# Kernel tuning notes

Measured on AMD Instinct MI355X. Metric: run time of the kernel, lower is better.

The kernel has to match this reference:

```python
import jax, jax.numpy as jnp
import numpy as np

B, N, K = 4, 4096, 16
EPS = 1e-12


def setup_inputs() -> dict:
    key = jax.random.key(0)
    k1, k2, k3 = jax.random.split(key, 3)
    ori = jax.random.normal(k1, (B, N, 3), dtype=jnp.float32)
    # adversarial cloud = original + small perturbation (realistic attack setting)
    adv = ori + 0.05 * jax.random.normal(k2, (B, N, 3), dtype=jnp.float32)
    nrm = jax.random.normal(k3, (B, N, 3), dtype=jnp.float32)
    nrm = nrm / (jnp.linalg.norm(nrm, axis=-1, keepdims=True) + EPS)  # unit normals
    return {"ori_pcs": ori, "adv_pcs": adv, "ori_normals": nrm, "k": K}


def _sqdist(a, b):
    # a: [B,N,3], b: [B,M,3] -> [B,N,M] squared euclidean distances (GEMM form)
    return ((a * a).sum(-1)[:, :, None] + (b * b).sum(-1)[:, None, :]
            - 2.0 * jnp.einsum('bnd,bmd->bnm', a, b))


def _gather_rows(pts, idx):
    # pts: [B,M,3], idx: [B,...] int -> [B,...,3]
    return jax.vmap(lambda p, i: p[i])(pts, idx)


def _kappa(pc, normals, k):
    # curvature proxy: mean |<normalized offset to kNN, normal>| per point -> [B,N]
    d = _sqdist(pc, pc)                       # [B,N,N]
    _, idx = jax.lax.top_k(-d, k + 1)         # nearest k+1 (incl. self)
    idx = idx[..., 1:]                        # drop self -> [B,N,k]
    nn = _gather_rows(pc, idx)                # [B,N,k,3]
    vec = nn - pc[:, :, None, :]
    vec = vec / (jnp.linalg.norm(vec, axis=-1, keepdims=True) + EPS)
    return jnp.abs(jnp.einsum('bnkd,bnd->bnk', vec, normals)).mean(-1)


def reference(ori_pcs, adv_pcs, ori_normals, k):
    # curvature of the clean cloud
    kappa_ori = _kappa(ori_pcs, ori_normals, k)            # [B,N]
    # adv points borrow the normal of their nearest original point
    d = _sqdist(adv_pcs, ori_pcs)                          # [B,N,N]
    nn_idx = jnp.argmin(d, axis=-1)                        # [B,N]
    adv_normals = _gather_rows(ori_normals, nn_idx)        # [B,N,3]
    kappa_adv = _kappa(adv_pcs, adv_normals, k)            # [B,N]
    # std of curvature over points (torch.std -> unbiased, ddof=1)
    std_ori = jnp.std(kappa_ori, axis=1, ddof=1)           # [B]
    std_adv = jnp.std(kappa_adv, axis=1, ddof=1)           # [B]
    return jnp.mean(jnp.abs(std_adv - std_ori))
```

## Files before the change

kernel.cpp:

```cpp
#include <hip/hip_runtime.h>
#include <math.h>

#define B_ 4
#define N_ 4096
#define K_ 16
#define WAVES 8
#define QPB (WAVES*2)
#define BPB (N_/QPB)
#define INF __builtin_huge_valf()

__device__ __forceinline__ float dpp_shr1_f(float x) {
    return __int_as_float(__builtin_amdgcn_update_dpp(
        __float_as_int(x), __float_as_int(x), 0x111, 0xF, 0xF, false));
}
__device__ __forceinline__ int dpp_shr1_i(int x) {
    return __builtin_amdgcn_update_dpp(x, x, 0x111, 0xF, 0xF, false);
}
__device__ __forceinline__ float readlane_f(float x, int l) {
    return __int_as_float(__builtin_amdgcn_readlane(__float_as_int(x), l));
}

#if __has_builtin(__builtin_amdgcn_inverse_ballot_w64)
#define LANEBIT(m, lane) __builtin_amdgcn_inverse_ballot_w64(m)
#else
#define LANEBIT(m, lane) ((((m) >> (lane)) & 1ull) != 0)
#endif

__global__ __launch_bounds__(512, 6) void curv_argmin_kernel(
    const float* __restrict__ ori, const float* __restrict__ adv,
    int* __restrict__ nnidx)
{
    __shared__ float2 sxy[N_];
    __shared__ float  sz[N_];
    const int tid = threadIdx.x, lane = tid & 63, w = tid >> 6;
    const int b  = blockIdx.x >> 8;
    const int qb = (blockIdx.x & 255) * QPB;
    const float* ob = ori + (size_t)b * (N_*3);
    const float* ab = adv + (size_t)b * (N_*3);
    for (int k = 0; k < N_/512; ++k) {
        int j = k*512 + tid;
        sxy[j] = make_float2(ob[3*j+0], ob[3*j+1]);
        sz[j]  = ob[3*j+2];
    }
    __syncthreads();

    const int n0 = qb + w*2, n1 = n0 + 1;
    const float m2x0 = -2.f*ab[3*n0+0], m2y0 = -2.f*ab[3*n0+1], m2z0 = -2.f*ab[3*n0+2];
    const float m2x1 = -2.f*ab[3*n1+0], m2y1 = -2.f*ab[3*n1+1], m2z1 = -2.f*ab[3*n1+2];

    float dm0 = INF, dm1 = INF; int jm0 = 0, jm1 = 0;
    for (int t = 0; t < N_/64; ++t) {
        int j = t*64 + lane;
        float2 p = sxy[j]; float pz = sz[j];
        float pp = fmaf(pz,pz, fmaf(p.y,p.y, p.x*p.x));
        float r0 = fmaf(pz,m2z0, fmaf(p.y,m2y0, fmaf(p.x,m2x0, pp)));
        float r1 = fmaf(pz,m2z1, fmaf(p.y,m2y1, fmaf(p.x,m2x1, pp)));
        if (r0 < dm0) { dm0 = r0; jm0 = j; }
        if (r1 < dm1) { dm1 = r1; jm1 = j; }
    }
    for (int s = 1; s < 64; s <<= 1) {
        float o0 = __shfl_xor(dm0, s); int a0 = __shfl_xor(jm0, s);
        float o1 = __shfl_xor(dm1, s); int a1 = __shfl_xor(jm1, s);
        if (o0 < dm0 || (o0 == dm0 && a0 < jm0)) { dm0 = o0; jm0 = a0; }
        if (o1 < dm1 || (o1 == dm1 && a1 < jm1)) { dm1 = o1; jm1 = a1; }
    }
    if (lane == 0) { nnidx[b*N_+n0] = jm0; nnidx[b*N_+n1] = jm1; }
}

__global__ __launch_bounds__(512, 6) void curv_kappa_kernel(
    const float* __restrict__ ori, const float* __restrict__ adv,
    const float* __restrict__ nrm, const int* __restrict__ nnidx,
    double* __restrict__ acc)
{
    __shared__ float2 sxy[N_];
    __shared__ float  sz[N_];
    __shared__ double rs[WAVES], rss[WAVES];
    const int tid = threadIdx.x, lane = tid & 63, w = tid >> 6;
    const int blk = blockIdx.x;
    const int job = blk >> 10;
    const int b   = (blk >> 8) & 3;
    const int qb  = (blk & 255) * QPB;

    const float* pb = (job ? adv : ori) + (size_t)b*(N_*3);
    const float* nb = nrm + (size_t)b*(N_*3);
    for (int k = 0; k < N_/512; ++k) {
        int j = k*512 + tid;
        sxy[j] = make_float2(pb[3*j+0], pb[3*j+1]);
        sz[j]  = pb[3*j+2];
    }
    __syncthreads();

    const int n0 = qb + w*2, n1 = n0 + 1;
    const float2 q0 = sxy[n0]; const float q0z = sz[n0];
    const float2 q1 = sxy[n1]; const float q1z = sz[n1];
    const float m2x0 = -2.f*q0.x, m2y0 = -2.f*q0.y, m2z0 = -2.f*q0z;
    const float m2x1 = -2.f*q1.x, m2y1 = -2.f*q1.y, m2z1 = -2.f*q1z;

    int nn0 = n0, nn1 = n1;
    if (job) { nn0 = nnidx[b*N_+n0]; nn1 = nnidx[b*N_+n1]; }
    const float nx0 = nb[3*nn0+0], ny0 = nb[3*nn0+1], nz0 = nb[3*nn0+2];
    const float nx1 = nb[3*nn1+0], ny1 = nb[3*nn1+1], nz1 = nb[3*nn1+2];

    const int selfT = n0 >> 6;

    float r0, r1; int i0 = lane, i1 = lane;
    {
        float2 p = sxy[lane]; float pz = sz[lane];
        float pp = fmaf(pz,pz, fmaf(p.y,p.y, p.x*p.x));
        r0 = fmaf(pz,m2z0, fmaf(p.y,m2y0, fmaf(p.x,m2x0, pp)));
        r1 = fmaf(pz,m2z1, fmaf(p.y,m2y1, fmaf(p.x,m2x1, pp)));
        if (selfT == 0) {
            if (lane == n0) r0 = INF;
            if (lane == n1) r1 = INF;
        }
    }
    #pragma unroll
    for (int k = 2; k <= 64; k <<= 1) {
        #pragma unroll
        for (int j = k >> 1; j > 0; j >>= 1) {
            bool sel = ((lane & k) == 0) == ((lane & j) == 0);
            float o0 = __shfl_xor(r0, j); int a0 = __shfl_xor(i0, j);
            float o1 = __shfl_xor(r1, j); int a1 = __shfl_xor(i1, j);
            if ((o0 < r0) == sel) { r0 = o0; i0 = a0; }
            if ((o1 < r1) == sel) { r1 = o1; i1 = a1; }
        }
    }
    float sd0 = r0, sd1 = r1; int si0 = i0, si1 = i1;
    float tau0 = readlane_f(sd0, 15), tau1 = readlane_f(sd1, 15);
    const int selfL0 = n0 & 63, selfL1 = n1 & 63;

    for (int t = 1; t < N_/64; ++t) {
        int j = t*64 + lane;
        float2 p = sxy[j]; float pz = sz[j];
        float pp = fmaf(pz,pz, fmaf(p.y,p.y, p.x*p.x));
        float d0 = fmaf(pz,m2z0, fmaf(p.y,m2y0, fmaf(p.x,m2x0, pp)));
        float d1 = fmaf(pz,m2z1, fmaf(p.y,m2y1, fmaf(p.x,m2x1, pp)));
        if (t == selfT) {
            if (lane == selfL0) d0 = INF;
            if (lane == selfL1) d1 = INF;
        }
        unsigned long long m0 = __ballot(d0 < tau0);
        if (m0) {
            do {
                int src = __builtin_ctzll(m0); m0 &= m0 - 1;
                float v = readlane_f(d0, src);
                int  vi = t*64 + src;
                bool gt = (sd0 > v);
                unsigned long long mg = __ballot(gt);
                float usd = dpp_shr1_f(sd0); int usi = dpp_shr1_i(si0);
                bool pg = LANEBIT(mg << 1, lane);
                sd0 = gt ? (pg ? usd : v ) : sd0;
                si0 = gt ? (pg ? usi : vi) : si0;
            } while (m0);
            tau0 = readlane_f(sd0, 15);
        }
        unsigned long long m1 = __ballot(d1 < tau1);
        if (m1) {
            do {
                int src = __builtin_ctzll(m1); m1 &= m1 - 1;
                float v = readlane_f(d1, src);
                int  vi = t*64 + src;
                bool gt = (sd1 > v);
                unsigned long long mg = __ballot(gt);
                float usd = dpp_shr1_f(sd1); int usi = dpp_shr1_i(si1);
                bool pg = LANEBIT(mg << 1, lane);
                sd1 = gt ? (pg ? usd : v ) : sd1;
                si1 = gt ? (pg ? usi : vi) : si1;
            } while (m1);
            tau1 = readlane_f(sd1, 15);
        }
    }

    float tl0 = 0.0f, tl1 = 0.0f;
    if (lane < K_) {
        {
            float2 p = sxy[si0]; float pz = sz[si0];
            float vx = p.x - q0.x, vy = p.y - q0.y, vz = pz - q0z;
            float L  = sqrtf(vx*vx + vy*vy + vz*vz) + 1e-12f;
            tl0 = fabsf(vx*nx0 + vy*ny0 + vz*nz0) / L;
        }
        {
            float2 p = sxy[si1]; float pz = sz[si1];
            float vx = p.x - q1.x, vy = p.y - q1.y, vz = pz - q1z;
            float L  = sqrtf(vx*vx + vy*vy + vz*vz) + 1e-12f;
            tl1 = fabsf(vx*nx1 + vy*ny1 + vz*nz1) / L;
        }
    }
    tl0 += __shfl_xor(tl0, 1); tl0 += __shfl_xor(tl0, 2);
    tl0 += __shfl_xor(tl0, 4); tl0 += __shfl_xor(tl0, 8);
    tl1 += __shfl_xor(tl1, 1); tl1 += __shfl_xor(tl1, 2);
    tl1 += __shfl_xor(tl1, 4); tl1 += __shfl_xor(tl1, 8);

    if (lane == 0) {
        double k0 = (double)tl0 * (1.0/16.0);
        double k1 = (double)tl1 * (1.0/16.0);
        rs[w]  = k0 + k1;
        rss[w] = k0*k0 + k1*k1;
    }
    __syncthreads();
    if (tid == 0) {
        double s = 0.0, ss = 0.0;
        #pragma unroll
        for (int i = 0; i < WAVES; ++i) { s += rs[i]; ss += rss[i]; }
        int row = job*4 + b;
        atomicAdd(&acc[row*2+0], s);
        atomicAdd(&acc[row*2+1], ss);
    }
}

__global__ void curv_finalize_kernel(const double* __restrict__ acc,
                                     float* __restrict__ out)
{
    if (threadIdx.x == 0 && blockIdx.x == 0) {
        double st[8];
        #pragma unroll
        for (int r = 0; r < 8; ++r) {
            double s   = acc[2*r+0];
            double ss  = acc[2*r+1];
            double var = (ss - s*s / (double)N_) / (double)(N_ - 1);
            st[r] = var > 0.0 ? sqrt(var) : 0.0;
        }
        double o = 0.0;
        #pragma unroll
        for (int bb = 0; bb < 4; ++bb) o += fabs(st[4+bb] - st[bb]);
        out[0] = (float)(o * 0.25);
    }
}

extern "C" void kernel_launch(void* const* d_in, const int* in_sizes, int n_in,
                              void* d_out, int out_size, void* d_ws, size_t ws_size,
                              hipStream_t stream)
{
    const float* ori = (const float*)d_in[0];
    const float* adv = (const float*)d_in[1];
    const float* nrm = (const float*)d_in[2];
    double* acc   = (double*)d_ws;
    int*    nnidx = (int*)((char*)d_ws + 128);
    float*  out   = (float*)d_out;

    hipMemsetAsync(acc, 0, 16 * sizeof(double), stream);
    curv_argmin_kernel<<<dim3(B_ * BPB), 512, 0, stream>>>(ori, adv, nnidx);
    curv_kappa_kernel<<<dim3(2 * B_ * BPB), 512, 0, stream>>>(ori, adv, nrm, nnidx, acc);
    curv_finalize_kernel<<<1, 64, 0, stream>>>(acc, out);
}
```

Before: 117.3 us.

## Sort points by z and prune kNN/argmin tiles via z-bound early exit

Adds a counting-sort kernel that buckets both clouds by z coordinate into a workspace, carrying each point's original index. The argmin and kNN kernels then scan 64-point tiles outward from the query's own tile, using per-tile prefix/suffix z bounds to stop once no remaining tile can beat the current best or k-th distance. This is meant to skip most of the all-pairs distance work, at the cost of an extra kernel, a fixed z range assumption in bucketing (clamped, so only sort quality suffers), and a small slack term in the pruning test.

```diff
diff --git a/kernel.cpp b/kernel.cpp
--- a/kernel.cpp
+++ b/kernel.cpp
@@ -7,7 +7,9 @@
 #define WAVES 8
 #define QPB (WAVES*2)
 #define BPB (N_/QPB)
+#define NBUCK 512
 #define INF __builtin_huge_valf()
+#define SLACK 1e-4f
 
 __device__ __forceinline__ float dpp_shr1_f(float x) {
     return __int_as_float(__builtin_amdgcn_update_dpp(
@@ -19,100 +21,227 @@
 __device__ __forceinline__ float readlane_f(float x, int l) {
     return __int_as_float(__builtin_amdgcn_readlane(__float_as_int(x), l));
 }
-
 #if __has_builtin(__builtin_amdgcn_inverse_ballot_w64)
 #define LANEBIT(m, lane) __builtin_amdgcn_inverse_ballot_w64(m)
 #else
 #define LANEBIT(m, lane) ((((m) >> (lane)) & 1ull) != 0)
 #endif
 
+#define POPS(m, dd, sdv, siv, tauv, tbase)                                 \
+    if (m) {                                                               \
+        do {                                                               \
+            int src = __builtin_ctzll(m); m &= m - 1;                      \
+            float v = readlane_f(dd, src);                                 \
+            int  vi = (tbase) + src;                                       \
+            bool gt = (sdv > v);                                           \
+            unsigned long long mg = __ballot(gt);                          \
+            float usd = dpp_shr1_f(sdv); int usi = dpp_shr1_i(siv);        \
+            bool pg = LANEBIT(mg << 1, lane);                              \
+            sdv = gt ? (pg ? usd : v ) : sdv;                              \
+            siv = gt ? (pg ? usi : vi) : siv;                              \
+        } while (m);                                                       \
+        tauv = readlane_f(sdv, 15);                                        \
+    }
+
+__global__ __launch_bounds__(512) void sortz_kernel(
+    const float* __restrict__ ori, const float* __restrict__ adv,
+    float4* __restrict__ gs)
+{
+    __shared__ int hist[NBUCK];
+    __shared__ int base[NBUCK];
+    __shared__ unsigned short sbuck[N_];
+    const int tid = threadIdx.x;
+    const int set = blockIdx.x >> 2;
+    const int b   = blockIdx.x & 3;
+    const float* src = (set ? adv : ori) + (size_t)b * (N_*3);
+    float4* dst = gs + (size_t)blockIdx.x * N_;
+
+    hist[tid] = 0;
+    __syncthreads();
+    #pragma unroll
+    for (int k = 0; k < N_/512; ++k) {
+        int j = k*512 + tid;
+        float z = src[3*j+2];
+        int bu = (int)((z + 4.25f) * (NBUCK/8.5f));
+        bu = bu < 0 ? 0 : (bu > NBUCK-1 ? NBUCK-1 : bu);
+        sbuck[j] = (unsigned short)bu;
+        atomicAdd(&hist[bu], 1);
+    }
+    __syncthreads();
+    int v = hist[tid];
+    for (int s = 1; s < NBUCK; s <<= 1) {
+        base[tid] = v; __syncthreads();
+        if (tid >= s) v += base[tid - s];
+        __syncthreads();
+    }
+    base[tid] = v - hist[tid];
+    hist[tid] = 0;
+    __syncthreads();
+    #pragma unroll
+    for (int k = 0; k < N_/512; ++k) {
+        int j = k*512 + tid;
+        int bu = sbuck[j];
+        int pos = base[bu] + atomicAdd(&hist[bu], 1);
+        dst[pos] = make_float4(src[3*j+0], src[3*j+1], src[3*j+2],
+                               __int_as_float(j));
+    }
+}
+
+#define STAGE_AND_STATS(gsrc)                                              \
+    _Pragma("unroll")                                                      \
+    for (int k = 0; k < N_/512; ++k) {                                     \
+        int j = k*512 + tid;                                               \
+        float4 f = (gsrc)[j];                                              \
+        sxy[j] = make_float2(f.x, f.y);                                    \
+        szs[j] = f.z;                                                      \
+    }                                                                      \
+    __syncthreads();                                                       \
+    _Pragma("unroll")                                                      \
+    for (int i = 0; i < 8; ++i) {                                          \
+        int t = w*8 + i;                                                   \
+        float zv = szs[t*64 + lane];                                       \
+        float mn = zv, mx = zv;                                            \
+        _Pragma("unroll")                                                  \
+        for (int s = 1; s < 64; s <<= 1) {                                 \
+            mn = fminf(mn, __shfl_xor(mn, s));                             \
+            mx = fmaxf(mx, __shfl_xor(mx, s));                             \
+        }                                                                  \
+        if (lane == 0) { tmn[t] = mn; tmx[t] = mx; }                       \
+    }                                                                      \
+    __syncthreads();                                                       \
+    if (w == 0) {                                                          \
+        float a = tmn[lane], c = tmx[lane];                                \
+        _Pragma("unroll")                                                  \
+        for (int s = 1; s < 64; s <<= 1) {                                 \
+            float u = __shfl_down(a, s); if (lane + s < 64) a = fminf(a,u);\
+            float u2 = __shfl_up(c, s);  if (lane >= s)     c = fmaxf(c,u2);\
+        }                                                                  \
+        sufmn[lane] = a; prfmx[lane] = c;                                  \
+    }                                                                      \
+    __syncthreads();
+
 __global__ __launch_bounds__(512, 6) void curv_argmin_kernel(
-    const float* __restrict__ ori, const float* __restrict__ adv,
-    int* __restrict__ nnidx)
+    const float4* __restrict__ gs, int* __restrict__ nnidx)
 {
     __shared__ float2 sxy[N_];
-    __shared__ float  sz[N_];
+    __shared__ float  szs[N_];
+    __shared__ float  tmn[64], tmx[64], sufmn[64], prfmx[64];
     const int tid = threadIdx.x, lane = tid & 63, w = tid >> 6;
     const int b  = blockIdx.x >> 8;
     const int qb = (blockIdx.x & 255) * QPB;
-    const float* ob = ori + (size_t)b * (N_*3);
-    const float* ab = adv + (size_t)b * (N_*3);
-    for (int k = 0; k < N_/512; ++k) {
-        int j = k*512 + tid;
-        sxy[j] = make_float2(ob[3*j+0], ob[3*j+1]);
-        sz[j]  = ob[3*j+2];
-    }
-    __syncthreads();
-
-    const int n0 = qb + w*2, n1 = n0 + 1;
-    const float m2x0 = -2.f*ab[3*n0+0], m2y0 = -2.f*ab[3*n0+1], m2z0 = -2.f*ab[3*n0+2];
-    const float m2x1 = -2.f*ab[3*n1+0], m2y1 = -2.f*ab[3*n1+1], m2z1 = -2.f*ab[3*n1+2];
+    const float4* go = gs + (size_t)b * N_;
+    const float4* ga = gs + (size_t)(4 + b) * N_;
+
+    STAGE_AND_STATS(go)
+
+    const int sq0 = qb + w*2, sq1 = sq0 + 1;
+    float4 f0 = ga[sq0], f1 = ga[sq1];
+    const int n0 = __float_as_int(f0.w), n1 = __float_as_int(f1.w);
+    const float m2x0 = -2.f*f0.x, m2y0 = -2.f*f0.y, m2z0 = -2.f*f0.z;
+    const float m2x1 = -2.f*f1.x, m2y1 = -2.f*f1.y, m2z1 = -2.f*f1.z;
+    const float qq0 = fmaf(f0.z,f0.z, fmaf(f0.y,f0.y, f0.x*f0.x));
+    const float qq1 = fmaf(f1.z,f1.z, fmaf(f1.y,f1.y, f1.x*f1.x));
+    const float q0z = f0.z, q1z = f1.z;
+
+    int T0;
+    { int l = 0, h = 64;
+      while (h - l > 1) { int m = (l+h)>>1; T0 = m; if (sufmn[m] <= q0z) l = m; else h = m; }
+      T0 = l; }
 
     float dm0 = INF, dm1 = INF; int jm0 = 0, jm1 = 0;
-    for (int t = 0; t < N_/64; ++t) {
-        int j = t*64 + lane;
-        float2 p = sxy[j]; float pz = sz[j];
-        float pp = fmaf(pz,pz, fmaf(p.y,p.y, p.x*p.x));
-        float r0 = fmaf(pz,m2z0, fmaf(p.y,m2y0, fmaf(p.x,m2x0, pp)));
-        float r1 = fmaf(pz,m2z1, fmaf(p.y,m2y1, fmaf(p.x,m2x1, pp)));
-        if (r0 < dm0) { dm0 = r0; jm0 = j; }
-        if (r1 < dm1) { dm1 = r1; jm1 = j; }
-    }
+    float bm0 = INF, bm1 = INF;
+#define APROC(t)                                                           \
+    {   int j = (t)*64 + lane;                                             \
+        float2 p = sxy[j]; float pz = szs[j];                              \
+        float pp = fmaf(pz,pz, fmaf(p.y,p.y, p.x*p.x));                    \
+        float r0 = fmaf(pz,m2z0, fmaf(p.y,m2y0, fmaf(p.x,m2x0, pp)));      \
+        float r1 = fmaf(pz,m2z1, fmaf(p.y,m2y1, fmaf(p.x,m2x1, pp)));      \
+        if (r0 < dm0) { dm0 = r0; jm0 = j; }                               \
+        if (r1 < dm1) { dm1 = r1; jm1 = j; }                               \
+        float g0 = dm0, g1 = dm1;                                          \
+        _Pragma("unroll")                                                  \
+        for (int s = 1; s < 64; s <<= 1) {                                 \
+            g0 = fminf(g0, __shfl_xor(g0, s));                             \
+            g1 = fminf(g1, __shfl_xor(g1, s));                             \
+        }                                                                  \
+        bm0 = g0; bm1 = g1; }
+
+    APROC(T0)
+    int tup = T0 + 1, tdn = T0 - 1;
+    for (;;) {
+        bool go_up = false, go_dn = false;
+        if (tup < 64) {
+            float m = sufmn[tup];
+            float a0 = m - q0z, a1 = m - q1z;
+            go_up = !((a0 > 0.f) && (fmaf(a0,a0,-qq0) >= bm0 + SLACK)) ||
+                    !((a1 > 0.f) && (fmaf(a1,a1,-qq1) >= bm1 + SLACK));
+        }
+        if (tdn >= 0) {
+            float m = prfmx[tdn];
+            float a0 = q0z - m, a1 = q1z - m;
+            go_dn = !((a0 > 0.f) && (fmaf(a0,a0,-qq0) >= bm0 + SLACK)) ||
+                    !((a1 > 0.f) && (fmaf(a1,a1,-qq1) >= bm1 + SLACK));
+        }
+        if (go_up) { APROC(tup) ++tup; }
+        if (go_dn) { APROC(tdn) --tdn; }
+        if (!go_up && !go_dn) break;
+    }
+#undef APROC
+    #pragma unroll
     for (int s = 1; s < 64; s <<= 1) {
         float o0 = __shfl_xor(dm0, s); int a0 = __shfl_xor(jm0, s);
         float o1 = __shfl_xor(dm1, s); int a1 = __shfl_xor(jm1, s);
         if (o0 < dm0 || (o0 == dm0 && a0 < jm0)) { dm0 = o0; jm0 = a0; }
         if (o1 < dm1 || (o1 == dm1 && a1 < jm1)) { dm1 = o1; jm1 = a1; }
     }
-    if (lane == 0) { nnidx[b*N_+n0] = jm0; nnidx[b*N_+n1] = jm1; }
+    if (lane == 0) {
+        nnidx[b*N_ + n0] = __float_as_int(go[jm0].w);
+        nnidx[b*N_ + n1] = __float_as_int(go[jm1].w);
+    }
 }
 
 __global__ __launch_bounds__(512, 6) void curv_kappa_kernel(
-    const float* __restrict__ ori, const float* __restrict__ adv,
-    const float* __restrict__ nrm, const int* __restrict__ nnidx,
-    double* __restrict__ acc)
+    const float4* __restrict__ gs, const float* __restrict__ nrm,
+    const int* __restrict__ nnidx, double* __restrict__ acc)
 {
     __shared__ float2 sxy[N_];
-    __shared__ float  sz[N_];
+    __shared__ float  szs[N_];
+    __shared__ float  tmn[64], tmx[64], sufmn[64], prfmx[64];
     __shared__ double rs[WAVES], rss[WAVES];
     const int tid = threadIdx.x, lane = tid & 63, w = tid >> 6;
     const int blk = blockIdx.x;
     const int job = blk >> 10;
     const int b   = (blk >> 8) & 3;
     const int qb  = (blk & 255) * QPB;
-
-    const float* pb = (job ? adv : ori) + (size_t)b*(N_*3);
-    const float* nb = nrm + (size_t)b*(N_*3);
-    for (int k = 0; k < N_/512; ++k) {
-        int j = k*512 + tid;
-        sxy[j] = make_float2(pb[3*j+0], pb[3*j+1]);
-        sz[j]  = pb[3*j+2];
-    }
-    __syncthreads();
-
-    const int n0 = qb + w*2, n1 = n0 + 1;
-    const float2 q0 = sxy[n0]; const float q0z = sz[n0];
-    const float2 q1 = sxy[n1]; const float q1z = sz[n1];
-    const float m2x0 = -2.f*q0.x, m2y0 = -2.f*q0.y, m2z0 = -2.f*q0z;
-    const float m2x1 = -2.f*q1.x, m2y1 = -2.f*q1.y, m2z1 = -2.f*q1z;
+    const float4* g = gs + (size_t)(job*4 + b) * N_;
+    const float* nb = nrm + (size_t)b * (N_*3);
+
+    STAGE_AND_STATS(g)
+
+    const int sq0 = qb + w*2, sq1 = sq0 + 1;
+    float4 f0 = g[sq0], f1 = g[sq1];
+    const int n0 = __float_as_int(f0.w), n1 = __float_as_int(f1.w);
+    const float q0x=f0.x, q0y=f0.y, q0z=f0.z;
+    const float q1x=f1.x, q1y=f1.y, q1z=f1.z;
+    const float m2x0 = -2.f*q0x, m2y0 = -2.f*q0y, m2z0 = -2.f*q0z;
+    const float m2x1 = -2.f*q1x, m2y1 = -2.f*q1y, m2z1 = -2.f*q1z;
+    const float qq0 = fmaf(q0z,q0z, fmaf(q0y,q0y, q0x*q0x));
+    const float qq1 = fmaf(q1z,q1z, fmaf(q1y,q1y, q1x*q1x));
 
     int nn0 = n0, nn1 = n1;
     if (job) { nn0 = nnidx[b*N_+n0]; nn1 = nnidx[b*N_+n1]; }
     const float nx0 = nb[3*nn0+0], ny0 = nb[3*nn0+1], nz0 = nb[3*nn0+2];
     const float nx1 = nb[3*nn1+0], ny1 = nb[3*nn1+1], nz1 = nb[3*nn1+2];
 
-    const int selfT = n0 >> 6;
-
-    float r0, r1; int i0 = lane, i1 = lane;
+    const int T0 = sq0 >> 6;
+    float r0, r1; int i0 = T0*64 + lane, i1 = i0;
     {
-        float2 p = sxy[lane]; float pz = sz[lane];
+        float2 p = sxy[i0]; float pz = szs[i0];
         float pp = fmaf(pz,pz, fmaf(p.y,p.y, p.x*p.x));
         r0 = fmaf(pz,m2z0, fmaf(p.y,m2y0, fmaf(p.x,m2x0, pp)));
         r1 = fmaf(pz,m2z1, fmaf(p.y,m2y1, fmaf(p.x,m2x1, pp)));
-        if (selfT == 0) {
-            if (lane == n0) r0 = INF;
-            if (lane == n1) r1 = INF;
-        }
+        if (lane == (sq0 & 63)) r0 = INF;
+        if (lane == (sq1 & 63)) r1 = INF;
     }
     #pragma unroll
     for (int k = 2; k <= 64; k <<= 1) {
@@ -127,61 +256,50 @@
     }
     float sd0 = r0, sd1 = r1; int si0 = i0, si1 = i1;
     float tau0 = readlane_f(sd0, 15), tau1 = readlane_f(sd1, 15);
-    const int selfL0 = n0 & 63, selfL1 = n1 & 63;
-
-    for (int t = 1; t < N_/64; ++t) {
-        int j = t*64 + lane;
-        float2 p = sxy[j]; float pz = sz[j];
-        float pp = fmaf(pz,pz, fmaf(p.y,p.y, p.x*p.x));
-        float d0 = fmaf(pz,m2z0, fmaf(p.y,m2y0, fmaf(p.x,m2x0, pp)));
-        float d1 = fmaf(pz,m2z1, fmaf(p.y,m2y1, fmaf(p.x,m2x1, pp)));
-        if (t == selfT) {
-            if (lane == selfL0) d0 = INF;
-            if (lane == selfL1) d1 = INF;
-        }
-        unsigned long long m0 = __ballot(d0 < tau0);
-        if (m0) {
-            do {
-                int src = __builtin_ctzll(m0); m0 &= m0 - 1;
-                float v = readlane_f(d0, src);
-                int  vi = t*64 + src;
-                bool gt = (sd0 > v);
-                unsigned long long mg = __ballot(gt);
-                float usd = dpp_shr1_f(sd0); int usi = dpp_shr1_i(si0);
-                bool pg = LANEBIT(mg << 1, lane);
-                sd0 = gt ? (pg ? usd : v ) : sd0;
-                si0 = gt ? (pg ? usi : vi) : si0;
-            } while (m0);
-            tau0 = readlane_f(sd0, 15);
-        }
-        unsigned long long m1 = __ballot(d1 < tau1);
-        if (m1) {
-            do {
-                int src = __builtin_ctzll(m1); m1 &= m1 - 1;
-                float v = readlane_f(d1, src);
-                int  vi = t*64 + src;
-                bool gt = (sd1 > v);
-                unsigned long long mg = __ballot(gt);
-                float usd = dpp_shr1_f(sd1); int usi = dpp_shr1_i(si1);
-                bool pg = LANEBIT(mg << 1, lane);
-                sd1 = gt ? (pg ? usd : v ) : sd1;
-                si1 = gt ? (pg ? usi : vi) : si1;
-            } while (m1);
-            tau1 = readlane_f(sd1, 15);
-        }
-    }
+
+#define KPROC(t)                                                           \
+    {   int tb = (t)*64; int j = tb + lane;                                \
+        float2 p = sxy[j]; float pz = szs[j];                              \
+        float pp = fmaf(pz,pz, fmaf(p.y,p.y, p.x*p.x));                    \
+        float d0 = fmaf(pz,m2z0, fmaf(p.y,m2y0, fmaf(p.x,m2x0, pp)));      \
+        float d1 = fmaf(pz,m2z1, fmaf(p.y,m2y1, fmaf(p.x,m2x1, pp)));      \
+        unsigned long long m0 = __ballot(d0 < tau0);                       \
+        POPS(m0, d0, sd0, si0, tau0, tb)                                   \
+        unsigned long long m1 = __ballot(d1 < tau1);                       \
+        POPS(m1, d1, sd1, si1, tau1, tb) }
+
+    int tup = T0 + 1, tdn = T0 - 1;
+    for (;;) {
+        bool go_up = false, go_dn = false;
+        if (tup < 64) {
+            float m = sufmn[tup];
+            float a0 = m - q0z, a1 = m - q1z;
+            go_up = !((a0 > 0.f) && (fmaf(a0,a0,-qq0) >= tau0 + SLACK)) ||
+                    !((a1 > 0.f) && (fmaf(a1,a1,-qq1) >= tau1 + SLACK));
+        }
+        if (tdn >= 0) {
+            float m = prfmx[tdn];
+            float a0 = q0z - m, a1 = q1z - m;
+            go_dn = !((a0 > 0.f) && (fmaf(a0,a0,-qq0) >= tau0 + SLACK)) ||
+                    !((a1 > 0.f) && (fmaf(a1,a1,-qq1) >= tau1 + SLACK));
+        }
+        if (go_up) { KPROC(tup) ++tup; }
+        if (go_dn) { KPROC(tdn) --tdn; }
+        if (!go_up && !go_dn) break;
+    }
+#undef KPROC
 
     float tl0 = 0.0f, tl1 = 0.0f;
     if (lane < K_) {
         {
-            float2 p = sxy[si0]; float pz = sz[si0];
-            float vx = p.x - q0.x, vy = p.y - q0.y, vz = pz - q0z;
+            float2 p = sxy[si0]; float pz = szs[si0];
+            float vx = p.x - q0x, vy = p.y - q0y, vz = pz - q0z;
             float L  = sqrtf(vx*vx + vy*vy + vz*vz) + 1e-12f;
             tl0 = fabsf(vx*nx0 + vy*ny0 + vz*nz0) / L;
         }
         {
-            float2 p = sxy[si1]; float pz = sz[si1];
-            float vx = p.x - q1.x, vy = p.y - q1.y, vz = pz - q1z;
+            float2 p = sxy[si1]; float pz = szs[si1];
+            float vx = p.x - q1x, vy = p.y - q1y, vz = pz - q1z;
             float L  = sqrtf(vx*vx + vy*vy + vz*vz) + 1e-12f;
             tl1 = fabsf(vx*nx1 + vy*ny1 + vz*nz1) / L;
         }
@@ -235,11 +353,13 @@
     const float* adv = (const float*)d_in[1];
     const float* nrm = (const float*)d_in[2];
     double* acc   = (double*)d_ws;
-    int*    nnidx = (int*)((char*)d_ws + 128);
+    int*    nnidx = (int*)((char*)d_ws + 256);
+    float4* gs    = (float4*)((char*)d_ws + 256 + 65536);
     float*  out   = (float*)d_out;
 
     hipMemsetAsync(acc, 0, 16 * sizeof(double), stream);
-    curv_argmin_kernel<<<dim3(B_ * BPB), 512, 0, stream>>>(ori, adv, nnidx);
-    curv_kappa_kernel<<<dim3(2 * B_ * BPB), 512, 0, stream>>>(ori, adv, nrm, nnidx, acc);
+    sortz_kernel<<<8, 512, 0, stream>>>(ori, adv, gs);
+    curv_argmin_kernel<<<dim3(B_ * BPB), 512, 0, stream>>>(gs, nnidx);
+    curv_kappa_kernel<<<dim3(2 * B_ * BPB), 512, 0, stream>>>(gs, nrm, nnidx, acc);
     curv_finalize_kernel<<<1, 64, 0, stream>>>(acc, out);
 }
```

After: 123.0 us. 1.05x slower.

## Morton-sort points and prune kNN/argmin scans with per-tile bounding boxes

Applied to the files above, without the earlier changes.

Adds a kernel that bins each cloud into a 16^3 Morton grid and counting-sorts the points, storing original indices alongside the coordinates. The argmin and kNN kernels then compute an axis-aligned bounding box per 64-point tile and scan only tiles whose box distance falls below the current threshold plus a small slack. Each wave now handles four queries instead of two, with 1024-thread blocks. This replaces the full O(N^2) distance scan with a pruned search, at the cost of an extra sort launch, more complex control flow, and reliance on a fixed grid range and a float slack for correctness.

```diff
diff --git a/kernel.cpp b/kernel.cpp
--- a/kernel.cpp
+++ b/kernel.cpp
@@ -4,10 +4,9 @@
 #define B_ 4
 #define N_ 4096
 #define K_ 16
-#define WAVES 8
-#define QPB (WAVES*2)
-#define BPB (N_/QPB)
+#define NT 64
 #define INF __builtin_huge_valf()
+#define SLACK 1e-4f
 
 __device__ __forceinline__ float dpp_shr1_f(float x) {
     return __int_as_float(__builtin_amdgcn_update_dpp(
@@ -19,189 +18,368 @@
 __device__ __forceinline__ float readlane_f(float x, int l) {
     return __int_as_float(__builtin_amdgcn_readlane(__float_as_int(x), l));
 }
-
+__device__ __forceinline__ float rflf(float x) {
+    return __int_as_float(__builtin_amdgcn_readfirstlane(__float_as_int(x)));
+}
 #if __has_builtin(__builtin_amdgcn_inverse_ballot_w64)
 #define LANEBIT(m, lane) __builtin_amdgcn_inverse_ballot_w64(m)
 #else
 #define LANEBIT(m, lane) ((((m) >> (lane)) & 1ull) != 0)
 #endif
 
-__global__ __launch_bounds__(512, 6) void curv_argmin_kernel(
+#define POP1(mi, di, sdi, sii, tb)                                         \
+    {   int src = __builtin_ctzll(mi); mi &= mi - 1;                       \
+        float v = readlane_f(di, src);                                     \
+        int  vi = (tb) + src;                                              \
+        unsigned long long mg = __ballot(sdi > v);                         \
+        float usd = dpp_shr1_f(sdi); int usi = dpp_shr1_i(sii);            \
+        bool gt = LANEBIT(mg, lane);                                       \
+        bool pg = LANEBIT(mg << 1, lane);                                  \
+        sdi = gt ? (pg ? usd : v ) : sdi;                                  \
+        sii = gt ? (pg ? usi : vi) : sii; }
+
+__device__ __forceinline__ int spread4(int v) {
+    return (v & 1) | ((v & 2) << 2) | ((v & 4) << 4) | ((v & 8) << 6);
+}
+
+__global__ __launch_bounds__(1024) void morton_sort_kernel(
     const float* __restrict__ ori, const float* __restrict__ adv,
-    int* __restrict__ nnidx)
+    float4* __restrict__ gs)
+{
+    __shared__ int hist[4096];
+    __shared__ int wsum[1024];
+    const int tid = threadIdx.x;
+    const int set = blockIdx.x >> 2, b = blockIdx.x & 3;
+    const float* src = (set ? adv : ori) + (size_t)b * (N_*3);
+    float4* dst = gs + (size_t)blockIdx.x * N_;
+
+    #pragma unroll
+    for (int k = 0; k < 4; ++k) hist[k*1024 + tid] = 0;
+    __syncthreads();
+
+    float px[4], py[4], pz[4]; int code[4];
+    #pragma unroll
+    for (int k = 0; k < 4; ++k) {
+        int j = k*1024 + tid;
+        float x = src[3*j+0], y = src[3*j+1], z = src[3*j+2];
+        px[k] = x; py[k] = y; pz[k] = z;
+        int ix = (int)((x + 4.25f) * (16.0f/8.5f));
+        int iy = (int)((y + 4.25f) * (16.0f/8.5f));
+        int iz = (int)((z + 4.25f) * (16.0f/8.5f));
+        ix = ix < 0 ? 0 : (ix > 15 ? 15 : ix);
+        iy = iy < 0 ? 0 : (iy > 15 ? 15 : iy);
+        iz = iz < 0 ? 0 : (iz > 15 ? 15 : iz);
+        code[k] = (spread4(ix) << 2) | (spread4(iy) << 1) | spread4(iz);
+        atomicAdd(&hist[code[k]], 1);
+    }
+    __syncthreads();
+    const int h0 = hist[4*tid], h1 = hist[4*tid+1],
+              h2 = hist[4*tid+2], h3 = hist[4*tid+3];
+    const int s = h0 + h1 + h2 + h3;
+    wsum[tid] = s;
+    __syncthreads();
+    for (int st = 1; st < 1024; st <<= 1) {
+        int tmp = (tid >= st) ? wsum[tid - st] : 0;
+        __syncthreads();
+        wsum[tid] += tmp;
+        __syncthreads();
+    }
+    int eb = wsum[tid] - s;
+    hist[4*tid]   = eb;
+    hist[4*tid+1] = eb + h0;
+    hist[4*tid+2] = eb + h0 + h1;
+    hist[4*tid+3] = eb + h0 + h1 + h2;
+    __syncthreads();
+    #pragma unroll
+    for (int k = 0; k < 4; ++k) {
+        int j = k*1024 + tid;
+        int pos = atomicAdd(&hist[code[k]], 1);
+        dst[pos] = make_float4(px[k], py[k], pz[k], __int_as_float(j));
+    }
+}
+
+#define STAGE_AABB(gsrc)                                                   \
+    _Pragma("unroll")                                                      \
+    for (int k = 0; k < 4; ++k) {                                          \
+        int j = k*1024 + tid;                                              \
+        float4 f = (gsrc)[j];                                              \
+        sxy[j] = make_float2(f.x, f.y);                                    \
+        szs[j] = f.z;                                                      \
+    }                                                                      \
+    __syncthreads();                                                       \
+    _Pragma("unroll")                                                      \
+    for (int i = 0; i < 4; ++i) {                                          \
+        int t = w*4 + i;                                                   \
+        float2 pxy = sxy[t*64 + lane]; float pzz = szs[t*64 + lane];       \
+        float x0 = pxy.x, x1 = pxy.x, y0 = pxy.y, y1 = pxy.y;              \
+        float z0 = pzz, z1 = pzz;                                          \
+        _Pragma("unroll")                                                  \
+        for (int s2 = 1; s2 < 64; s2 <<= 1) {                              \
+            x0 = fminf(x0, __shfl_xor(x0, s2));                            \
+            x1 = fmaxf(x1, __shfl_xor(x1, s2));                            \
+            y0 = fminf(y0, __shfl_xor(y0, s2));                            \
+            y1 = fmaxf(y1, __shfl_xor(y1, s2));                            \
+            z0 = fminf(z0, __shfl_xor(z0, s2));                            \
+            z1 = fmaxf(z1, __shfl_xor(z1, s2));                            \
+        }                                                                  \
+        if (lane == 0) { alx[t]=x0; ahx[t]=x1; aly[t]=y0; ahy[t]=y1;       \
+                         alz[t]=z0; ahz[t]=z1; }                           \
+    }                                                                      \
+    __syncthreads();
+
+#define AABB2(qx,qy,qz)                                                    \
+    ({ float dx_ = fmaxf(fmaxf(t_lx - (qx), (qx) - t_hx), 0.f);            \
+       float dy_ = fmaxf(fmaxf(t_ly - (qy), (qy) - t_hy), 0.f);            \
+       float dz_ = fmaxf(fmaxf(t_lz - (qz), (qz) - t_hz), 0.f);            \
+       fmaf(dz_, dz_, fmaf(dy_, dy_, dx_*dx_)); })
+
+__global__ __launch_bounds__(1024, 4) void curv_argmin_kernel(
+    const float4* __restrict__ gs, int* __restrict__ nnidx)
 {
     __shared__ float2 sxy[N_];
-    __shared__ float  sz[N_];
+    __shared__ float  szs[N_];
+    __shared__ float alx[NT], ahx[NT], aly[NT], ahy[NT], alz[NT], ahz[NT];
     const int tid = threadIdx.x, lane = tid & 63, w = tid >> 6;
-    const int b  = blockIdx.x >> 8;
-    const int qb = (blockIdx.x & 255) * QPB;
-    const float* ob = ori + (size_t)b * (N_*3);
-    const float* ab = adv + (size_t)b * (N_*3);
-    for (int k = 0; k < N_/512; ++k) {
-        int j = k*512 + tid;
-        sxy[j] = make_float2(ob[3*j+0], ob[3*j+1]);
-        sz[j]  = ob[3*j+2];
-    }
-    __syncthreads();
-
-    const int n0 = qb + w*2, n1 = n0 + 1;
-    const float m2x0 = -2.f*ab[3*n0+0], m2y0 = -2.f*ab[3*n0+1], m2z0 = -2.f*ab[3*n0+2];
-    const float m2x1 = -2.f*ab[3*n1+0], m2y1 = -2.f*ab[3*n1+1], m2z1 = -2.f*ab[3*n1+2];
-
-    float dm0 = INF, dm1 = INF; int jm0 = 0, jm1 = 0;
-    for (int t = 0; t < N_/64; ++t) {
-        int j = t*64 + lane;
-        float2 p = sxy[j]; float pz = sz[j];
-        float pp = fmaf(pz,pz, fmaf(p.y,p.y, p.x*p.x));
-        float r0 = fmaf(pz,m2z0, fmaf(p.y,m2y0, fmaf(p.x,m2x0, pp)));
-        float r1 = fmaf(pz,m2z1, fmaf(p.y,m2y1, fmaf(p.x,m2x1, pp)));
-        if (r0 < dm0) { dm0 = r0; jm0 = j; }
-        if (r1 < dm1) { dm1 = r1; jm1 = j; }
-    }
-    for (int s = 1; s < 64; s <<= 1) {
-        float o0 = __shfl_xor(dm0, s); int a0 = __shfl_xor(jm0, s);
-        float o1 = __shfl_xor(dm1, s); int a1 = __shfl_xor(jm1, s);
-        if (o0 < dm0 || (o0 == dm0 && a0 < jm0)) { dm0 = o0; jm0 = a0; }
-        if (o1 < dm1 || (o1 == dm1 && a1 < jm1)) { dm1 = o1; jm1 = a1; }
-    }
-    if (lane == 0) { nnidx[b*N_+n0] = jm0; nnidx[b*N_+n1] = jm1; }
-}
-
-__global__ __launch_bounds__(512, 6) void curv_kappa_kernel(
-    const float* __restrict__ ori, const float* __restrict__ adv,
-    const float* __restrict__ nrm, const int* __restrict__ nnidx,
-    double* __restrict__ acc)
+    const int b = blockIdx.x >> 6, m = blockIdx.x & 63;
+    const float4* go = gs + (size_t)b * N_;
+    const float4* ga = gs + (size_t)(4 + b) * N_;
+
+    STAGE_AABB(go)
+
+    const int sq0 = (w*64 + m) * 4;
+    float4 f0 = ga[sq0+0], f1 = ga[sq0+1], f2 = ga[sq0+2], f3 = ga[sq0+3];
+    const float q0x=rflf(f0.x), q0y=rflf(f0.y), q0z=rflf(f0.z);
+    const float q1x=rflf(f1.x), q1y=rflf(f1.y), q1z=rflf(f1.z);
+    const float q2x=rflf(f2.x), q2y=rflf(f2.y), q2z=rflf(f2.z);
+    const float q3x=rflf(f3.x), q3y=rflf(f3.y), q3z=rflf(f3.z);
+    const int n0 = __builtin_amdgcn_readfirstlane(__float_as_int(f0.w));
+    const int n1 = __builtin_amdgcn_readfirstlane(__float_as_int(f1.w));
+    const int n2 = __builtin_amdgcn_readfirstlane(__float_as_int(f2.w));
+    const int n3 = __builtin_amdgcn_readfirstlane(__float_as_int(f3.w));
+    const float m2x0=-2.f*q0x, m2y0=-2.f*q0y, m2z0=-2.f*q0z;
+    const float m2x1=-2.f*q1x, m2y1=-2.f*q1y, m2z1=-2.f*q1z;
+    const float m2x2=-2.f*q2x, m2y2=-2.f*q2y, m2z2=-2.f*q2z;
+    const float m2x3=-2.f*q3x, m2y3=-2.f*q3y, m2z3=-2.f*q3z;
+    const float qq0 = fmaf(q0z,q0z, fmaf(q0y,q0y, q0x*q0x));
+    const float qq1 = fmaf(q1z,q1z, fmaf(q1y,q1y, q1x*q1x));
+    const float qq2 = fmaf(q2z,q2z, fmaf(q2y,q2y, q2x*q2x));
+    const float qq3 = fmaf(q3z,q3z, fmaf(q3y,q3y, q3x*q3x));
+
+    const float t_lx = alx[lane], t_hx = ahx[lane];
+    const float t_ly = aly[lane], t_hy = ahy[lane];
+    const float t_lz = alz[lane], t_hz = ahz[lane];
+    float ad0 = AABB2(q0x,q0y,q0z), ad1 = AABB2(q1x,q1y,q1z);
+    float ad2 = AABB2(q2x,q2y,q2z), ad3 = AABB2(q3x,q3y,q3z);
+
+    float v0=ad0, v1=ad1, v2=ad2, v3=ad3; int l0=lane,l1=lane,l2=lane,l3=lane;
+    #pragma unroll
+    for (int s2 = 1; s2 < 64; s2 <<= 1) {
+        { float ov=__shfl_xor(v0,s2); int ol=__shfl_xor(l0,s2);
+          if (ov<v0 || (ov==v0 && ol<l0)) { v0=ov; l0=ol; } }
+        { float ov=__shfl_xor(v1,s2); int ol=__shfl_xor(l1,s2);
+          if (ov<v1 || (ov==v1 && ol<l1)) { v1=ov; l1=ol; } }
+        { float ov=__shfl_xor(v2,s2); int ol=__shfl_xor(l2,s2);
+          if (ov<v2 || (ov==v2 && ol<l2)) { v2=ov; l2=ol; } }
+        { float ov=__shfl_xor(v3,s2); int ol=__shfl_xor(l3,s2);
+          if (ov<v3 || (ov==v3 && ol<l3)) { v3=ov; l3=ol; } }
+    }
+    unsigned long long scanned =
+        (1ull << __builtin_amdgcn_readfirstlane(l0)) |
+        (1ull << __builtin_amdgcn_readfirstlane(l1)) |
+        (1ull << __builtin_amdgcn_readfirstlane(l2)) |
+        (1ull << __builtin_amdgcn_readfirstlane(l3));
+
+    float dm0=INF,dm1=INF,dm2=INF,dm3=INF; int jm0=0,jm1=0,jm2=0,jm3=0;
+#define ASCAN(t)                                                           \
+    {   int j = (t)*64 + lane;                                             \
+        float2 p = sxy[j]; float pz2 = szs[j];                             \
+        float pp = fmaf(pz2,pz2, fmaf(p.y,p.y, p.x*p.x));                  \
+        float r0 = fmaf(pz2,m2z0, fmaf(p.y,m2y0, fmaf(p.x,m2x0, pp)));     \
+        float r1 = fmaf(pz2,m2z1, fmaf(p.y,m2y1, fmaf(p.x,m2x1, pp)));     \
+        float r2 = fmaf(pz2,m2z2, fmaf(p.y,m2y2, fmaf(p.x,m2x2, pp)));     \
+        float r3 = fmaf(pz2,m2z3, fmaf(p.y,m2y3, fmaf(p.x,m2x3, pp)));     \
+        if (r0 < dm0) { dm0 = r0; jm0 = j; }                               \
+        if (r1 < dm1) { dm1 = r1; jm1 = j; }                               \
+        if (r2 < dm2) { dm2 = r2; jm2 = j; }                               \
+        if (r3 < dm3) { dm3 = r3; jm3 = j; }  }
+    { unsigned long long cm = scanned;
+      while (cm) { int t = __builtin_ctzll(cm); cm &= cm-1; ASCAN(t) } }
+
+    float bm0=dm0, bm1=dm1, bm2=dm2, bm3=dm3;
+    #pragma unroll
+    for (int s2 = 1; s2 < 64; s2 <<= 1) {
+        bm0 = fminf(bm0, __shfl_xor(bm0, s2));
+        bm1 = fminf(bm1, __shfl_xor(bm1, s2));
+        bm2 = fminf(bm2, __shfl_xor(bm2, s2));
+        bm3 = fminf(bm3, __shfl_xor(bm3, s2));
+    }
+    float bt0 = bm0 + qq0 + SLACK, bt1 = bm1 + qq1 + SLACK;
+    float bt2 = bm2 + qq2 + SLACK, bt3 = bm3 + qq3 + SLACK;
+    unsigned long long cm =
+        ( __ballot(ad0 < bt0) | __ballot(ad1 < bt1)
+        | __ballot(ad2 < bt2) | __ballot(ad3 < bt3) ) & ~scanned;
+    while (cm) { int t = __builtin_ctzll(cm); cm &= cm-1; ASCAN(t) }
+#undef ASCAN
+
+    #pragma unroll
+    for (int s2 = 1; s2 < 64; s2 <<= 1) {
+        { float od=__shfl_xor(dm0,s2); int oj=__shfl_xor(jm0,s2);
+          if (od<dm0 || (od==dm0 && oj<jm0)) { dm0=od; jm0=oj; } }
+        { float od=__shfl_xor(dm1,s2); int oj=__shfl_xor(jm1,s2);
+          if (od<dm1 || (od==dm1 && oj<jm1)) { dm1=od; jm1=oj; } }
+        { float od=__shfl_xor(dm2,s2); int oj=__shfl_xor(jm2,s2);
+          if (od<dm2 || (od==dm2 && oj<jm2)) { dm2=od; jm2=oj; } }
+        { float od=__shfl_xor(dm3,s2); int oj=__shfl_xor(jm3,s2);
+          if (od<dm3 || (od==dm3 && oj<jm3)) { dm3=od; jm3=oj; } }
+    }
+    if (lane == 0) {
+        nnidx[b*N_ + n0] = __float_as_int(go[jm0].w);
+        nnidx[b*N_ + n1] = __float_as_int(go[jm1].w);
+        nnidx[b*N_ + n2] = __float_as_int(go[jm2].w);
+        nnidx[b*N_ + n3] = __float_as_int(go[jm3].w);
+    }
+}
+
+__global__ __launch_bounds__(1024, 8) void curv_kappa_kernel(
+    const float4* __restrict__ gs, const float* __restrict__ nrm,
+    const int* __restrict__ nnidx, double* __restrict__ acc)
 {
     __shared__ float2 sxy[N_];
-    __shared__ float  sz[N_];
-    __shared__ double rs[WAVES], rss[WAVES];
+    __shared__ float  szs[N_];
+    __shared__ float alx[NT], ahx[NT], aly[NT], ahy[NT], alz[NT], ahz[NT];
+    __shared__ double rs[16], rss[16];
     const int tid = threadIdx.x, lane = tid & 63, w = tid >> 6;
     const int blk = blockIdx.x;
-    const int job = blk >> 10;
-    const int b   = (blk >> 8) & 3;
-    const int qb  = (blk & 255) * QPB;
-
-    const float* pb = (job ? adv : ori) + (size_t)b*(N_*3);
-    const float* nb = nrm + (size_t)b*(N_*3);
-    for (int k = 0; k < N_/512; ++k) {
-        int j = k*512 + tid;
-        sxy[j] = make_float2(pb[3*j+0], pb[3*j+1]);
-        sz[j]  = pb[3*j+2];
-    }
-    __syncthreads();
-
-    const int n0 = qb + w*2, n1 = n0 + 1;
-    const float2 q0 = sxy[n0]; const float q0z = sz[n0];
-    const float2 q1 = sxy[n1]; const float q1z = sz[n1];
-    const float m2x0 = -2.f*q0.x, m2y0 = -2.f*q0.y, m2z0 = -2.f*q0z;
-    const float m2x1 = -2.f*q1.x, m2y1 = -2.f*q1.y, m2z1 = -2.f*q1z;
-
-    int nn0 = n0, nn1 = n1;
-    if (job) { nn0 = nnidx[b*N_+n0]; nn1 = nnidx[b*N_+n1]; }
-    const float nx0 = nb[3*nn0+0], ny0 = nb[3*nn0+1], nz0 = nb[3*nn0+2];
-    const float nx1 = nb[3*nn1+0], ny1 = nb[3*nn1+1], nz1 = nb[3*nn1+2];
-
-    const int selfT = n0 >> 6;
-
-    float r0, r1; int i0 = lane, i1 = lane;
+    const int job = blk >> 8;
+    const int b   = (blk >> 6) & 3;
+    const int m   = blk & 63;
+    const float4* g  = gs + (size_t)(job*4 + b) * N_;
+    const float* nb  = nrm + (size_t)b * (N_*3);
+
+    STAGE_AABB(g)
+
+    const int sq0 = (w*64 + m) * 4;
+    const int T0  = sq0 >> 6;
+    float4 f0 = g[sq0+0], f1 = g[sq0+1], f2 = g[sq0+2], f3 = g[sq0+3];
+    const float q0x=rflf(f0.x), q0y=rflf(f0.y), q0z=rflf(f0.z);
+    const float q1x=rflf(f1.x), q1y=rflf(f1.y), q1z=rflf(f1.z);
+    const float q2x=rflf(f2.x), q2y=rflf(f2.y), q2z=rflf(f2.z);
+    const float q3x=rflf(f3.x), q3y=rflf(f3.y), q3z=rflf(f3.z);
+    const int n0 = __builtin_amdgcn_readfirstlane(__float_as_int(f0.w));
+    const int n1 = __builtin_amdgcn_readfirstlane(__float_as_int(f1.w));
+    const int n2 = __builtin_amdgcn_readfirstlane(__float_as_int(f2.w));
+    const int n3 = __builtin_amdgcn_readfirstlane(__float_as_int(f3.w));
+    const int nn0 = job ? nnidx[b*N_ + n0] : n0;
+    const int nn1 = job ? nnidx[b*N_ + n1] : n1;
+    const int nn2 = job ? nnidx[b*N_ + n2] : n2;
+    const int nn3 = job ? nnidx[b*N_ + n3] : n3;
+    const float nx0=rflf(nb[3*nn0+0]), ny0=rflf(nb[3*nn0+1]), nz0=rflf(nb[3*nn0+2]);
+    const float nx1=rflf(nb[3*nn1+0]), ny1=rflf(nb[3*nn1+1]), nz1=rflf(nb[3*nn1+2]);
+    const float nx2=rflf(nb[3*nn2+0]), ny2=rflf(nb[3*nn2+1]), nz2=rflf(nb[3*nn2+2]);
+    const float nx3=rflf(nb[3*nn3+0]), ny3=rflf(nb[3*nn3+1]), nz3=rflf(nb[3*nn3+2]);
+    const float m2x0=-2.f*q0x, m2y0=-2.f*q0y, m2z0=-2.f*q0z;
+    const float m2x1=-2.f*q1x, m2y1=-2.f*q1y, m2z1=-2.f*q1z;
+    const float m2x2=-2.f*q2x, m2y2=-2.f*q2y, m2z2=-2.f*q2z;
+    const float m2x3=-2.f*q3x, m2y3=-2.f*q3y, m2z3=-2.f*q3z;
+    const float qq0 = fmaf(q0z,q0z, fmaf(q0y,q0y, q0x*q0x));
+    const float qq1 = fmaf(q1z,q1z, fmaf(q1y,q1y, q1x*q1x));
+    const float qq2 = fmaf(q2z,q2z, fmaf(q2y,q2y, q2x*q2x));
+    const float qq3 = fmaf(q3z,q3z, fmaf(q3y,q3y, q3x*q3x));
+
+    const float t_lx = alx[lane], t_hx = ahx[lane];
+    const float t_ly = aly[lane], t_hy = ahy[lane];
+    const float t_lz = alz[lane], t_hz = ahz[lane];
+    float ad0 = AABB2(q0x,q0y,q0z), ad1 = AABB2(q1x,q1y,q1z);
+    float ad2 = AABB2(q2x,q2y,q2z), ad3 = AABB2(q3x,q3y,q3z);
+
+    const int j0 = T0*64 + lane;
+    float sd0, sd1, sd2, sd3;
+    int   si0 = j0, si1 = j0, si2 = j0, si3 = j0;
     {
-        float2 p = sxy[lane]; float pz = sz[lane];
-        float pp = fmaf(pz,pz, fmaf(p.y,p.y, p.x*p.x));
-        r0 = fmaf(pz,m2z0, fmaf(p.y,m2y0, fmaf(p.x,m2x0, pp)));
-        r1 = fmaf(pz,m2z1, fmaf(p.y,m2y1, fmaf(p.x,m2x1, pp)));
-        if (selfT == 0) {
-            if (lane == n0) r0 = INF;
-            if (lane == n1) r1 = INF;
-        }
+        float2 p = sxy[j0]; float pz0 = szs[j0];
+        float pp = fmaf(pz0,pz0, fmaf(p.y,p.y, p.x*p.x));
+        sd0 = fmaf(pz0,m2z0, fmaf(p.y,m2y0, fmaf(p.x,m2x0, pp)));
+        sd1 = fmaf(pz0,m2z1, fmaf(p.y,m2y1, fmaf(p.x,m2x1, pp)));
+        sd2 = fmaf(pz0,m2z2, fmaf(p.y,m2y2, fmaf(p.x,m2x2, pp)));
+        sd3 = fmaf(pz0,m2z3, fmaf(p.y,m2y3, fmaf(p.x,m2x3, pp)));
+        const int sl = sq0 & 63;
+        if (lane == sl    ) sd0 = INF;
+        if (lane == sl + 1) sd1 = INF;
+        if (lane == sl + 2) sd2 = INF;
+        if (lane == sl + 3) sd3 = INF;
     }
     #pragma unroll
     for (int k = 2; k <= 64; k <<= 1) {
         #pragma unroll
-        for (int j = k >> 1; j > 0; j >>= 1) {
-            bool sel = ((lane & k) == 0) == ((lane & j) == 0);
-            float o0 = __shfl_xor(r0, j); int a0 = __shfl_xor(i0, j);
-            float o1 = __shfl_xor(r1, j); int a1 = __shfl_xor(i1, j);
-            if ((o0 < r0) == sel) { r0 = o0; i0 = a0; }
-            if ((o1 < r1) == sel) { r1 = o1; i1 = a1; }
+        for (int jj = k >> 1; jj > 0; jj >>= 1) {
+            bool sel = ((lane & k) == 0) == ((lane & jj) == 0);
+            { float o=__shfl_xor(sd0,jj); int a=__shfl_xor(si0,jj);
+              if ((o<sd0)==sel) { sd0=o; si0=a; } }
+            { float o=__shfl_xor(sd1,jj); int a=__shfl_xor(si1,jj);
+              if ((o<sd1)==sel) { sd1=o; si1=a; } }
+            { float o=__shfl_xor(sd2,jj); int a=__shfl_xor(si2,jj);
+              if ((o<sd2)==sel) { sd2=o; si2=a; } }
+            { float o=__shfl_xor(sd3,jj); int a=__shfl_xor(si3,jj);
+              if ((o<sd3)==sel) { sd3=o; si3=a; } }
         }
     }
-    float sd0 = r0, sd1 = r1; int si0 = i0, si1 = i1;
     float tau0 = readlane_f(sd0, 15), tau1 = readlane_f(sd1, 15);
-    const int selfL0 = n0 & 63, selfL1 = n1 & 63;
-
-    for (int t = 1; t < N_/64; ++t) {
-        int j = t*64 + lane;
-        float2 p = sxy[j]; float pz = sz[j];
-        float pp = fmaf(pz,pz, fmaf(p.y,p.y, p.x*p.x));
-        float d0 = fmaf(pz,m2z0, fmaf(p.y,m2y0, fmaf(p.x,m2x0, pp)));
-        float d1 = fmaf(pz,m2z1, fmaf(p.y,m2y1, fmaf(p.x,m2x1, pp)));
-        if (t == selfT) {
-            if (lane == selfL0) d0 = INF;
-            if (lane == selfL1) d1 = INF;
+    float tau2 = readlane_f(sd2, 15), tau3 = readlane_f(sd3, 15);
+
+    float tq0 = tau0 + qq0 + SLACK, tq1 = tau1 + qq1 + SLACK;
+    float tq2 = tau2 + qq2 + SLACK, tq3 = tau3 + qq3 + SLACK;
+    unsigned long long cm =
+        ( __ballot(ad0 < tq0) | __ballot(ad1 < tq1)
+        | __ballot(ad2 < tq2) | __ballot(ad3 < tq3) ) & ~(1ull << T0);
+
+    while (cm) {
+        int t = __builtin_ctzll(cm); cm &= cm - 1;
+        int tb = t*64, j = tb + lane;
+        float2 p = sxy[j]; float pz2 = szs[j];
+        float pp = fmaf(pz2,pz2, fmaf(p.y,p.y, p.x*p.x));
+        float d0 = fmaf(pz2,m2z0, fmaf(p.y,m2y0, fmaf(p.x,m2x0, pp)));
+        float d1 = fmaf(pz2,m2z1, fmaf(p.y,m2y1, fmaf(p.x,m2x1, pp)));
+        float d2 = fmaf(pz2,m2z2, fmaf(p.y,m2y2, fmaf(p.x,m2x2, pp)));
+        float d3 = fmaf(pz2,m2z3, fmaf(p.y,m2y3, fmaf(p.x,m2x3, pp)));
+        unsigned long long m0 = __ballot(d0 < tau0);
+        unsigned long long m1 = __ballot(d1 < tau1);
+        unsigned long long m2 = __ballot(d2 < tau2);
+        unsigned long long m3 = __ballot(d3 < tau3);
+        while (m0 | m1 | m2 | m3) {
+            if (m0) POP1(m0, d0, sd0, si0, tb)
+            if (m1) POP1(m1, d1, sd1, si1, tb)
+            if (m2) POP1(m2, d2, sd2, si2, tb)
+            if (m3) POP1(m3, d3, sd3, si3, tb)
         }
-        unsigned long long m0 = __ballot(d0 < tau0);
-        if (m0) {
-            do {
-                int src = __builtin_ctzll(m0); m0 &= m0 - 1;
-                float v = readlane_f(d0, src);
-                int  vi = t*64 + src;
-                bool gt = (sd0 > v);
-                unsigned long long mg = __ballot(gt);
-                float usd = dpp_shr1_f(sd0); int usi = dpp_shr1_i(si0);
-                bool pg = LANEBIT(mg << 1, lane);
-                sd0 = gt ? (pg ? usd : v ) : sd0;
-                si0 = gt ? (pg ? usi : vi) : si0;
-            } while (m0);
-            tau0 = readlane_f(sd0, 15);
-        }
-        unsigned long long m1 = __ballot(d1 < tau1);
-        if (m1) {
-            do {
-                int src = __builtin_ctzll(m1); m1 &= m1 - 1;
-                float v = readlane_f(d1, src);
-                int  vi = t*64 + src;
-                bool gt = (sd1 > v);
-                unsigned long long mg = __ballot(gt);
-                float usd = dpp_shr1_f(sd1); int usi = dpp_shr1_i(si1);
-                bool pg = LANEBIT(mg << 1, lane);
-                sd1 = gt ? (pg ? usd : v ) : sd1;
-                si1 = gt ? (pg ? usi : vi) : si1;
-            } while (m1);
-            tau1 = readlane_f(sd1, 15);
-        }
-    }
-
-    float tl0 = 0.0f, tl1 = 0.0f;
-    if (lane < K_) {
-        {
-            float2 p = sxy[si0]; float pz = sz[si0];
-            float vx = p.x - q0.x, vy = p.y - q0.y, vz = pz - q0z;
-            float L  = sqrtf(vx*vx + vy*vy + vz*vz) + 1e-12f;
-            tl0 = fabsf(vx*nx0 + vy*ny0 + vz*nz0) / L;
-        }
-        {
-            float2 p = sxy[si1]; float pz = sz[si1];
-            float vx = p.x - q1.x, vy = p.y - q1.y, vz = pz - q1z;
-            float L  = sqrtf(vx*vx + vy*vy + vz*vz) + 1e-12f;
-            tl1 = fabsf(vx*nx1 + vy*ny1 + vz*nz1) / L;
-        }
-    }
-    tl0 += __shfl_xor(tl0, 1); tl0 += __shfl_xor(tl0, 2);
-    tl0 += __shfl_xor(tl0, 4); tl0 += __shfl_xor(tl0, 8);
-    tl1 += __shfl_xor(tl1, 1); tl1 += __shfl_xor(tl1, 2);
-    tl1 += __shfl_xor(tl1, 4); tl1 += __shfl_xor(tl1, 8);
-
-    if (lane == 0) {
-        double k0 = (double)tl0 * (1.0/16.0);
-        double k1 = (double)tl1 * (1.0/16.0);
-        rs[w]  = k0 + k1;
-        rss[w] = k0*k0 + k1*k1;
-    }
+        tau0 = readlane_f(sd0, 15); tau1 = readlane_f(sd1, 15);
+        tau2 = readlane_f(sd2, 15); tau3 = readlane_f(sd3, 15);
+    }
+
+    double ksum = 0.0, kss = 0.0;
+#define KTAIL(siN, qxN, qyN, qzN, nxN, nyN, nzN)                           \
+    {   float tl = 0.0f;                                                   \
+        if (lane < K_) {                                                   \
+            float2 p = sxy[siN]; float pz2 = szs[siN];                     \
+            float vx = p.x - qxN, vy = p.y - qyN, vz = pz2 - qzN;          \
+            float L  = sqrtf(vx*vx + vy*vy + vz*vz) + 1e-12f;              \
+            tl = fabsf(fmaf(vz,nzN, fmaf(vy,nyN, vx*nxN))) / L;            \
+        }                                                                  \
+        tl += __shfl_xor(tl, 1); tl += __shfl_xor(tl, 2);                  \
+        tl += __shfl_xor(tl, 4); tl += __shfl_xor(tl, 8);                  \
+        if (lane == 0) { double kk = (double)tl * (1.0/16.0);              \
+                         ksum += kk; kss += kk*kk; } }
+    KTAIL(si0, q0x, q0y, q0z, nx0, ny0, nz0)
+    KTAIL(si1, q1x, q1y, q1z, nx1, ny1, nz1)
+    KTAIL(si2, q2x, q2y, q2z, nx2, ny2, nz2)
+    KTAIL(si3, q3x, q3y, q3z, nx3, ny3, nz3)
+#undef KTAIL
+
+    if (lane == 0) { rs[w] = ksum; rss[w] = kss; }
     __syncthreads();
     if (tid == 0) {
         double s = 0.0, ss = 0.0;
         #pragma unroll
-        for (int i = 0; i < WAVES; ++i) { s += rs[i]; ss += rss[i]; }
+        for (int i = 0; i < 16; ++i) { s += rs[i]; ss += rss[i]; }
         int row = job*4 + b;
         atomicAdd(&acc[row*2+0], s);
         atomicAdd(&acc[row*2+1], ss);
@@ -235,11 +413,13 @@
     const float* adv = (const float*)d_in[1];
     const float* nrm = (const float*)d_in[2];
     double* acc   = (double*)d_ws;
-    int*    nnidx = (int*)((char*)d_ws + 128);
+    int*    nnidx = (int*)((char*)d_ws + 256);
+    float4* gs    = (float4*)((char*)d_ws + 256 + 65536);
     float*  out   = (float*)d_out;
 
     hipMemsetAsync(acc, 0, 16 * sizeof(double), stream);
-    curv_argmin_kernel<<<dim3(B_ * BPB), 512, 0, stream>>>(ori, adv, nnidx);
-    curv_kappa_kernel<<<dim3(2 * B_ * BPB), 512, 0, stream>>>(ori, adv, nrm, nnidx, acc);
+    morton_sort_kernel<<<8, 1024, 0, stream>>>(ori, adv, gs);
+    curv_argmin_kernel<<<B_ * 64, 1024, 0, stream>>>(gs, nnidx);
+    curv_kappa_kernel<<<2 * B_ * 64, 1024, 0, stream>>>(gs, nrm, nnidx, acc);
     curv_finalize_kernel<<<1, 64, 0, stream>>>(acc, out);
 }
```

Measured after the change: 167.7 us. +43.0%, slower.
